# Performance work log

Measured on AMD Instinct MI355X. Metric: run time of the kernel, lower is better.

## Reference

```python
import jax, jax.numpy as jnp
import numpy as np

SH_DIM = 9                      # (sh_deg+1)^2, sh_deg=2
DATA_DIM = SH_DIM * 3 + 1       # 28
FINE = 8
COARSE = 32
RADIUS = 1.3
NUM_ATOMS = 16
BATCH = 128
STEP = (RADIUS * 2.0 / COARSE / FINE) / 2.0   # fine_voxel_len / 2
N_INTRS = COARSE * 3 * 2 * FINE               # 1536


def sh_encode(dirs):
    # degree-2 real spherical harmonics bases, [.., 9]
    x, y, z = dirs[..., 0], dirs[..., 1], dirs[..., 2]
    C0 = 0.28209479177387814
    C1 = 0.4886025119029199
    C2 = (1.0925484305920792, -1.0925484305920792, 0.31539156525252005,
          -1.0925484305920792, 0.5462742152960396)
    return jnp.stack([
        jnp.full_like(x, C0), -C1 * y, C1 * z, -C1 * x,
        C2[0] * x * y, C2[1] * y * z, C2[2] * (2.0 * z * z - x * x - y * y),
        C2[3] * x * z, C2[4] * (x * x - y * y)], axis=-1)


def dict_interp(grid, atoms, pts):
    # pts: [N,3] normalized to [0,1). grid: [COARSE^3, A]. atoms: [FINE^3, A, D].
    # coarse voxel -> dictionary coefficients; trilinear interp of atoms inside it.
    cpos = pts * COARSE
    cidx = jnp.clip(jnp.floor(cpos), 0, COARSE - 1)
    ci = cidx.astype(jnp.int32)
    coeff = grid[(ci[:, 0] * COARSE + ci[:, 1]) * COARSE + ci[:, 2]]  # [N, A]
    local = cpos - cidx                       # [0,1) within coarse voxel
    fpos = local * FINE - 0.5
    f0f = jnp.floor(fpos)
    w = fpos - f0f                            # trilinear weights
    f0 = f0f.astype(jnp.int32)
    out = jnp.zeros((pts.shape[0], DATA_DIM), dtype=pts.dtype)
    for dx in (0, 1):
        for dy in (0, 1):
            for dz in (0, 1):
                ix = jnp.clip(f0[:, 0] + dx, 0, FINE - 1)
                iy = jnp.clip(f0[:, 1] + dy, 0, FINE - 1)
                iz = jnp.clip(f0[:, 2] + dz, 0, FINE - 1)
                wt = ((w[:, 0] if dx else 1.0 - w[:, 0]) *
                      (w[:, 1] if dy else 1.0 - w[:, 1]) *
                      (w[:, 2] if dz else 1.0 - w[:, 2]))
                vals = jnp.einsum('na,nad->nd', coeff, atoms[(ix * FINE + iy) * FINE + iz])
                out = out + wt[:, None] * vals
    return out


def setup_inputs() -> dict:
    key = jax.random.key(0)
    k1, k2, k3, k4 = jax.random.split(key, 4)
    rays_o = jnp.array([0.0, 0.0, -2.0 * RADIUS]) + 0.05 * jax.random.normal(k1, (BATCH, 3), jnp.float32)
    d = 0.25 * jax.random.normal(k2, (BATCH, 3), jnp.float32) + jnp.array([0.0, 0.0, 1.0])
    rays_d = d / jnp.linalg.norm(d, axis=-1, keepdims=True)
    grid = 0.01 * jax.random.normal(k3, (COARSE ** 3, NUM_ATOMS), jnp.float32)
    atoms_sh = jax.random.uniform(k4, (FINE ** 3, NUM_ATOMS, DATA_DIM - 1), jnp.float32)
    atoms = jnp.concatenate([atoms_sh, jnp.full((FINE ** 3, NUM_ATOMS, 1), 0.01, jnp.float32)], -1)
    return {"rays_o": rays_o, "rays_d": rays_d, "grid": grid, "atoms": atoms, "grid_id": 0}


def reference(rays_o, rays_d, grid, atoms, grid_id):
    B = rays_o.shape[0]
    # ---- sample_proposal (no-grad in original) ----
    off_pos = (RADIUS - rays_o) / rays_d
    off_neg = (-RADIUS - rays_o) / rays_d
    start = jnp.max(jnp.minimum(off_pos, off_neg), axis=-1, keepdims=True)
    steps = jnp.arange(N_INTRS, dtype=rays_o.dtype)[None, :]
    intersections = jax.lax.stop_gradient(start + steps * STEP)        # [B, 1536]
    tsec = intersections[:, :-1]                                       # [B, M]
    M = N_INTRS - 1
    pts = rays_o[:, None, :] + tsec[:, :, None] * rays_d[:, None, :]   # [B, M, 3]
    mask = jnp.all((pts > -RADIUS) & (pts < RADIUS), axis=-1)          # [B, M]
    pts_n = jnp.clip((pts + RADIUS) / (2.0 * RADIUS), 0.0, 1.0 - 1e-6)
    pts_n = jax.lax.stop_gradient(pts_n).reshape(-1, 3)
    # ---- dictionary interpolation (computed densely, zeroed by mask) ----
    data = dict_interp(grid, atoms, pts_n).reshape(B, M, DATA_DIM)
    sigma = jax.nn.relu(jnp.where(mask, data[..., -1], 0.0))           # [B, M]
    # ---- sigma -> alpha / weights ----
    dists = (intersections[:, 1:] - intersections[:, :-1]) * jnp.linalg.norm(rays_d, axis=-1, keepdims=True)
    alpha = 1.0 - jnp.exp(-sigma * dists)
    trans = jnp.concatenate([jnp.ones((B, 1), alpha.dtype),
                             jnp.cumprod(1.0 - alpha + 1e-10, axis=-1)[:, :-1]], axis=-1)
    abs_light = alpha * trans                                          # [B, M]
    # ---- SH -> rgb, composite ----
    sh_mult = sh_encode(rays_d)[:, None, None, :]                      # [B,1,1,9]
    sh = data[..., :-1].reshape(B, M, 3, SH_DIM)
    rgb_raw = jnp.where(mask[..., None], jnp.sum(sh_mult * sh, axis=-1), 0.0)  # [B,M,3]
    rgb = jnp.sum(abs_light[..., None] * jax.nn.sigmoid(rgb_raw), axis=1)
    rgb = rgb + (1.0 - jnp.sum(abs_light, axis=-1))[:, None]           # white background
    depth = jnp.sum(abs_light * tsec, axis=-1)
    return rgb, alpha, depth
```

## Files before the change

### kernel.cpp

```cpp
#include <hip/hip_runtime.h>

typedef unsigned int u32;

#define MSAMP 1535
#define NS 1024
#define RADF 1.3f
#define STEPF ((float)(1.3 * 2.0 / 32.0 / 8.0 / 2.0))
#define NATOMS 229376
#define NCELLG 32768
#define CSCALE 0.06f

#if __has_builtin(__builtin_amdgcn_sdot4)
#define SDOT4(a, b, c) __builtin_amdgcn_sdot4((a), (b), (c), false)
#else
static __device__ __forceinline__ int SDOT4(int a, int b, int c) {
#pragma unroll
    for (int i = 0; i < 4; i++) {
        int ai = (a << (24 - 8 * i)) >> 24;
        int bi = (b << (24 - 8 * i)) >> 24;
        c += ai * bi;
    }
    return c;
}
#endif

__device__ __forceinline__ u32 q4(float a, float b, float c, float d, float S) {
    int i0 = (int)rintf(fminf(fmaxf(a * S, -127.0f), 127.0f));
    int i1 = (int)rintf(fminf(fmaxf(b * S, -127.0f), 127.0f));
    int i2 = (int)rintf(fminf(fmaxf(c * S, -127.0f), 127.0f));
    int i3 = (int)rintf(fminf(fmaxf(d * S, -127.0f), 127.0f));
    return (u32)(i0 & 255) | ((u32)(i1 & 255) << 8) | ((u32)(i2 & 255) << 16)
         | ((u32)(i3 & 255) << 24);
}

__global__ __launch_bounds__(256) void k_t(const float* __restrict__ atoms,
                                           const float* __restrict__ grid,
                                           signed char* __restrict__ wst2,
                                           uint4* __restrict__ gridq,
                                           float4* __restrict__ acc4) {
    int o = blockIdx.x * 256 + threadIdx.x;
    if (o < NATOMS) {
        float v = atoms[o];
        int cell = o / 448;
        int r = o - cell * 448;
        int a = r / 28;
        int d = r - a * 28;
        int s = d >> 2, j = d & 3;
        int qv = (int)rintf(v * 127.0f);
        wst2[s * 32768 + cell * 64 + j * 16 + a] = (signed char)qv;
    } else if (o < NATOMS + NCELLG) {
        int cell = o - NATOMS;
        const float4* gp = (const float4*)(grid + cell * 16);
        float4 c0 = gp[0], c1 = gp[1], c2 = gp[2], c3 = gp[3];
        const float S = 127.0f / CSCALE;
        uint4 outv;
        outv.x = q4(c0.x, c0.y, c0.z, c0.w, S);
        outv.y = q4(c1.x, c1.y, c1.z, c1.w, S);
        outv.z = q4(c2.x, c2.y, c2.z, c2.w, S);
        outv.w = q4(c3.x, c3.y, c3.z, c3.w, S);
        gridq[cell] = outv;
    } else {
        acc4[o - NATOMS - NCELLG] = make_float4(0.0f, 0.0f, 0.0f, 0.0f);
    }
}

__global__ __launch_bounds__(512) void k_p1(const float* __restrict__ ro,
                                            const float* __restrict__ rd,
                                            const uint4* __restrict__ gridq,
                                            const signed char* __restrict__ wst2,
                                            float* __restrict__ acc4) {
    __shared__ __align__(16) signed char hl[512 * 80];
    int bx = blockIdx.x;
    int s  = bx >> 6;
    int pr = bx & 63;
    int tid = threadIdx.x;
    int ray = pr * 2 + (tid >> 8);
    int q   = tid & 255;

    {
        const uint4* src = (const uint4*)(wst2 + s * 32768);
#pragma unroll
        for (int it = 0; it < 4; it++) {
            int idx = it * 512 + tid;
            uint4 v = src[idx];
            int cell = idx >> 2, part = idx & 3;
            *(uint4*)&hl[cell * 80 + part * 16] = v;
        }
    }
    __syncthreads();

    float ox = ro[ray * 3 + 0], oy = ro[ray * 3 + 1], oz = ro[ray * 3 + 2];
    float dx = rd[ray * 3 + 0], dy = rd[ray * 3 + 1], dz = rd[ray * 3 + 2];
    float a0 = ( RADF - ox) / dx, b0 = (-RADF - ox) / dx;
    float a1 = ( RADF - oy) / dy, b1 = (-RADF - oy) / dy;
    float a2 = ( RADF - oz) / dz, b2 = (-RADF - oz) / dz;
    float st = fmaxf(fmaxf(fminf(a0, b0), fminf(a1, b1)), fminf(a2, b2));

    float shm[9];
    shm[0] = 0.28209479177387814f;
    shm[1] = -0.4886025119029199f * dy;
    shm[2] =  0.4886025119029199f * dz;
    shm[3] = -0.4886025119029199f * dx;
    shm[4] =  1.0925484305920792f * dx * dy;
    shm[5] = -1.0925484305920792f * dy * dz;
    shm[6] =  0.31539156525252005f * (2.0f * dz * dz - dx * dx - dy * dy);
    shm[7] = -1.0925484305920792f * dx * dz;
    shm[8] =  0.5462742152960396f * (dx * dx - dy * dy);

    float wA[4] = {0,0,0,0}, wB[4] = {0,0,0,0};
    int chanA = 0, chanB = 0; bool hasB = false;
    switch (s) {
        case 0: chanA=0; wA[0]=shm[0]; wA[1]=shm[1]; wA[2]=shm[2]; wA[3]=shm[3]; break;
        case 1: chanA=0; wA[0]=shm[4]; wA[1]=shm[5]; wA[2]=shm[6]; wA[3]=shm[7]; break;
        case 2: chanA=0; wA[0]=shm[8];
                chanB=1; wB[1]=shm[0]; wB[2]=shm[1]; wB[3]=shm[2]; hasB=true; break;
        case 3: chanA=1; wA[0]=shm[3]; wA[1]=shm[4]; wA[2]=shm[5]; wA[3]=shm[6]; break;
        case 4: chanA=1; wA[0]=shm[7]; wA[1]=shm[8];
                chanB=2; wB[2]=shm[0]; wB[3]=shm[1]; hasB=true; break;
        case 5: chanA=2; wA[0]=shm[2]; wA[1]=shm[3]; wA[2]=shm[4]; wA[3]=shm[5]; break;
        default: chanA=2; wA[0]=shm[6]; wA[1]=shm[7]; wA[2]=shm[8];
                chanB=3; wB[3]=1.0f; hasB=true; break;
    }
    const float QS = CSCALE / (127.0f * 127.0f);
#pragma unroll
    for (int i = 0; i < 4; i++) { wA[i] *= QS; wB[i] *= QS; }

#pragma unroll
    for (int k = 0; k < 4; k++) {
        int m = q + k * 256;
        float t = st + (float)m * STEPF;
        float px = ox + t * dx, py = oy + t * dy, pz = oz + t * dz;
        bool inb = (px > -RADF) && (px < RADF) && (py > -RADF) && (py < RADF)
                && (pz > -RADF) && (pz < RADF);
        if (!inb) continue;

        const float inv2R = 1.0f / 2.6f;
        float pnx = fminf(fmaxf((px + RADF) * inv2R, 0.0f), 0.999999f);
        float pny = fminf(fmaxf((py + RADF) * inv2R, 0.0f), 0.999999f);
        float pnz = fminf(fmaxf((pz + RADF) * inv2R, 0.0f), 0.999999f);

        float cpx = pnx * 32.0f, cpy = pny * 32.0f, cpz = pnz * 32.0f;
        float cfx = floorf(cpx), cfy = floorf(cpy), cfz = floorf(cpz);
        int cix = (int)cfx, ciy = (int)cfy, ciz = (int)cfz;

        float fpx = (cpx - cfx) * 8.0f - 0.5f;
        float fpy = (cpy - cfy) * 8.0f - 0.5f;
        float fpz = (cpz - cfz) * 8.0f - 0.5f;
        float ffx = floorf(fpx), ffy = floorf(fpy), ffz = floorf(fpz);
        int f0x = (int)ffx, f0y = (int)ffy, f0z = (int)ffz;
        float wx = fpx - ffx, wy = fpy - ffy, wz = fpz - ffz;

        int ixa[2] = { max(f0x, 0), min(f0x + 1, 7) };
        int iya[2] = { max(f0y, 0), min(f0y + 1, 7) };
        int iza[2] = { max(f0z, 0), min(f0z + 1, 7) };
        float wxa[2] = { 1.0f - wx, wx };
        float wya[2] = { 1.0f - wy, wy };
        float wza[2] = { 1.0f - wz, wz };

        uint4 cq = gridq[(cix * 32 + ciy) * 32 + ciz];
        float acc[4] = {0.0f, 0.0f, 0.0f, 0.0f};

#pragma unroll
        for (int cx = 0; cx < 2; cx++)
#pragma unroll
        for (int cy = 0; cy < 2; cy++)
#pragma unroll
        for (int cz = 0; cz < 2; cz++) {
            float wt = wxa[cx] * wya[cy] * wza[cz];
            int cb = ((ixa[cx] * 8 + iya[cy]) * 8 + iza[cz]) * 80;
#pragma unroll
            for (int j = 0; j < 4; j++) {
                uint4 qa = *(const uint4*)&hl[cb + j * 16];
                int di = SDOT4((int)qa.x, (int)cq.x, 0);
                di = SDOT4((int)qa.y, (int)cq.y, di);
                di = SDOT4((int)qa.z, (int)cq.z, di);
                di = SDOT4((int)qa.w, (int)cq.w, di);
                acc[j] = fmaf(wt, (float)di, acc[j]);
            }
        }

        float vA = fmaf(wA[0], acc[0], fmaf(wA[1], acc[1],
                   fmaf(wA[2], acc[2], wA[3] * acc[3])));
        int base = (ray * NS + m) * 4;
        atomicAdd(&acc4[base + chanA], vA);
        if (hasB) {
            float vB = fmaf(wB[0], acc[0], fmaf(wB[1], acc[1],
                       fmaf(wB[2], acc[2], wB[3] * acc[3])));
            atomicAdd(&acc4[base + chanB], vB);
        }
    }
}

__global__ __launch_bounds__(1024) void k_p2(const float* __restrict__ ro,
                                             const float* __restrict__ rd,
                                             const float4* __restrict__ acc4,
                                             float* __restrict__ rgb_out,
                                             float* __restrict__ alpha_out,
                                             float* __restrict__ depth_out) {
    int ray = blockIdx.x;
    int t = threadIdx.x;
    int lane = t & 63, wave = t >> 6;

    int abase = ray * MSAMP;
    if (NS + t < MSAMP) alpha_out[abase + NS + t] = 0.0f;

    float dx = rd[ray * 3 + 0], dy = rd[ray * 3 + 1], dz = rd[ray * 3 + 2];
    float ox = ro[ray * 3 + 0], oy = ro[ray * 3 + 1], oz = ro[ray * 3 + 2];
    float a0 = ( RADF - ox) / dx, b0 = (-RADF - ox) / dx;
    float a1 = ( RADF - oy) / dy, b1 = (-RADF - oy) / dy;
    float a2 = ( RADF - oz) / dz, b2 = (-RADF - oz) / dz;
    float st = fmaxf(fmaxf(fminf(a0, b0), fminf(a1, b1)), fminf(a2, b2));
    float nrm = sqrtf(dx * dx + dy * dy + dz * dz);

    int m = t;
    float tm = st + (float)m * STEPF;
    float4 d4 = acc4[ray * NS + m];
    float sigma = fmaxf(d4.w, 0.0f);
    float alpha = 1.0f - __expf(-sigma * STEPF * nrm);
    float r0 = 1.0f / (1.0f + __expf(-d4.x));
    float r1 = 1.0f / (1.0f + __expf(-d4.y));
    float r2 = 1.0f / (1.0f + __expf(-d4.z));
    alpha_out[abase + m] = alpha;

    float p = 1.0f - alpha + 1e-10f;

    float incl = p;
#pragma unroll
    for (int off = 1; off < 64; off <<= 1) {
        float vv = __shfl_up(incl, off);
        if (lane >= off) incl *= vv;
    }
    __shared__ float wprod[16];
    if (lane == 63) wprod[wave] = incl;
    __syncthreads();
    float excl = __shfl_up(incl, 1);
    if (lane == 0) excl = 1.0f;
    for (int w = 0; w < 16; w++) if (w < wave) excl *= wprod[w];

    float w_ = alpha * excl;
    float vals[5] = { w_ * r0, w_ * r1, w_ * r2, w_ * tm, w_ };
    __shared__ float wred[16][5];
#pragma unroll
    for (int i = 0; i < 5; i++) {
        float v = vals[i];
        v += __shfl_xor(v, 1);  v += __shfl_xor(v, 2);  v += __shfl_xor(v, 4);
        v += __shfl_xor(v, 8);  v += __shfl_xor(v, 16); v += __shfl_xor(v, 32);
        if (lane == 0) wred[wave][i] = v;
    }
    __syncthreads();
    if (t == 0) {
        float res[5];
#pragma unroll
        for (int i = 0; i < 5; i++) {
            float r_ = 0.0f;
            for (int w = 0; w < 16; w++) r_ += wred[w][i];
            res[i] = r_;
        }
        float omw = 1.0f - res[4];
        rgb_out[ray * 3 + 0] = res[0] + omw;
        rgb_out[ray * 3 + 1] = res[1] + omw;
        rgb_out[ray * 3 + 2] = res[2] + omw;
        depth_out[ray] = res[3];
    }
}

extern "C" void kernel_launch(void* const* d_in, const int* in_sizes, int n_in,
                              void* d_out, int out_size, void* d_ws, size_t ws_size,
                              hipStream_t stream) {
    const float* ro    = (const float*)d_in[0];
    const float* rd    = (const float*)d_in[1];
    const float* grid  = (const float*)d_in[2];
    const float* atoms = (const float*)d_in[3];
    int B = in_sizes[0] / 3;

    signed char* wst2 = (signed char*)d_ws;
    uint4* gridq = (uint4*)((char*)d_ws + 229376);
    float* acc4  = (float*)((char*)d_ws + 229376 + 524288);

    float* out       = (float*)d_out;
    float* rgb_out   = out;
    float* alpha_out = out + B * 3;
    float* depth_out = out + B * 3 + B * MSAMP;

    hipLaunchKernelGGL(k_t,  dim3(393216 / 256), dim3(256), 0, stream,
                       atoms, grid, wst2, (uint4*)gridq, (float4*)acc4);
    hipLaunchKernelGGL(k_p1, dim3(448), dim3(512), 0, stream,
                       ro, rd, (const uint4*)gridq, wst2, acc4);
    hipLaunchKernelGGL(k_p2, dim3(B), dim3(1024), 0, stream,
                       ro, rd, (const float4*)acc4, rgb_out, alpha_out, depth_out);
}
```

Before: 83.17 us.

## Fold per-ray SH projection into atoms and fuse interpolation with compositing

New measurement: 74.84 us. 1.11x faster.

```diff
diff --git a/kernel.cpp b/kernel.cpp
--- a/kernel.cpp
+++ b/kernel.cpp
@@ -6,9 +6,9 @@
 #define NS 1024
 #define RADF 1.3f
 #define STEPF ((float)(1.3 * 2.0 / 32.0 / 8.0 / 2.0))
-#define NATOMS 229376
 #define NCELLG 32768
 #define CSCALE 0.06f
+#define PRANGE 4.0f
 
 #if __has_builtin(__builtin_amdgcn_sdot4)
 #define SDOT4(a, b, c) __builtin_amdgcn_sdot4((a), (b), (c), false)
@@ -33,23 +33,55 @@
          | ((u32)(i3 & 255) << 24);
 }
 
-__global__ __launch_bounds__(256) void k_t(const float* __restrict__ atoms,
-                                           const float* __restrict__ grid,
-                                           signed char* __restrict__ wst2,
-                                           uint4* __restrict__ gridq,
-                                           float4* __restrict__ acc4) {
-    int o = blockIdx.x * 256 + threadIdx.x;
-    if (o < NATOMS) {
-        float v = atoms[o];
-        int cell = o / 448;
-        int r = o - cell * 448;
-        int a = r / 28;
-        int d = r - a * 28;
-        int s = d >> 2, j = d & 3;
-        int qv = (int)rintf(v * 127.0f);
-        wst2[s * 32768 + cell * 64 + j * 16 + a] = (signed char)qv;
-    } else if (o < NATOMS + NCELLG) {
-        int cell = o - NATOMS;
+__global__ __launch_bounds__(256) void k_prep(const float* __restrict__ rd,
+                                              const float* __restrict__ atoms,
+                                              const float* __restrict__ grid,
+                                              uint4* __restrict__ Pq,
+                                              uint4* __restrict__ gridq) {
+    __shared__ __align__(16) float af[448];
+    int b = blockIdx.x, t = threadIdx.x;
+    if (b < 512) {
+        if (t < 112) ((float4*)af)[t] = ((const float4*)(atoms + b * 448))[t];
+        int r = t & 127;
+        float dx = rd[r * 3 + 0], dy = rd[r * 3 + 1], dz = rd[r * 3 + 2];
+        float shm[9];
+        shm[0] = 0.28209479177387814f;
+        shm[1] = -0.4886025119029199f * dy;
+        shm[2] =  0.4886025119029199f * dz;
+        shm[3] = -0.4886025119029199f * dx;
+        shm[4] =  1.0925484305920792f * dx * dy;
+        shm[5] = -1.0925484305920792f * dy * dz;
+        shm[6] =  0.31539156525252005f * (2.0f * dz * dz - dx * dx - dy * dy);
+        shm[7] = -1.0925484305920792f * dx * dz;
+        shm[8] =  0.5462742152960396f * (dx * dx - dy * dy);
+        __syncthreads();
+#pragma unroll
+        for (int iter = 0; iter < 2; iter++) {
+            int ch = (t >> 7) + 2 * iter;
+            u32 w[4] = {0u, 0u, 0u, 0u};
+            if (ch < 3) {
+                const float S = 127.0f / PRANGE;
+#pragma unroll
+                for (int a = 0; a < 16; a++) {
+                    const float* ap = af + a * 28 + ch * 9;
+                    float p = shm[0] * ap[0];
+#pragma unroll
+                    for (int k = 1; k < 9; k++) p = fmaf(shm[k], ap[k], p);
+                    int q = (int)rintf(fminf(fmaxf(p * S, -127.0f), 127.0f));
+                    w[a >> 2] |= ((u32)(q & 255)) << (8 * (a & 3));
+                }
+            } else {
+#pragma unroll
+                for (int a = 0; a < 16; a++) {
+                    float p = af[a * 28 + 27];
+                    int q = (int)rintf(fminf(fmaxf(p * 127.0f, -127.0f), 127.0f));
+                    w[a >> 2] |= ((u32)(q & 255)) << (8 * (a & 3));
+                }
+            }
+            Pq[b * 512 + r * 4 + ch] = make_uint4(w[0], w[1], w[2], w[3]);
+        }
+    } else {
+        int cell = (b - 512) * 256 + t;
         const float4* gp = (const float4*)(grid + cell * 16);
         float4 c0 = gp[0], c1 = gp[1], c2 = gp[2], c3 = gp[3];
         const float S = 127.0f / CSCALE;
@@ -59,35 +91,33 @@
         outv.z = q4(c2.x, c2.y, c2.z, c2.w, S);
         outv.w = q4(c3.x, c3.y, c3.z, c3.w, S);
         gridq[cell] = outv;
-    } else {
-        acc4[o - NATOMS - NCELLG] = make_float4(0.0f, 0.0f, 0.0f, 0.0f);
-    }
-}
-
-__global__ __launch_bounds__(512) void k_p1(const float* __restrict__ ro,
-                                            const float* __restrict__ rd,
-                                            const uint4* __restrict__ gridq,
-                                            const signed char* __restrict__ wst2,
-                                            float* __restrict__ acc4) {
+    }
+}
+
+__global__ __launch_bounds__(1024) void k_main(const float* __restrict__ ro,
+                                               const float* __restrict__ rd,
+                                               const uint4* __restrict__ gridq,
+                                               const uint4* __restrict__ Pq,
+                                               float* __restrict__ rgb_out,
+                                               float* __restrict__ alpha_out,
+                                               float* __restrict__ depth_out) {
     __shared__ __align__(16) signed char hl[512 * 80];
-    int bx = blockIdx.x;
-    int s  = bx >> 6;
-    int pr = bx & 63;
-    int tid = threadIdx.x;
-    int ray = pr * 2 + (tid >> 8);
-    int q   = tid & 255;
-
-    {
-        const uint4* src = (const uint4*)(wst2 + s * 32768);
-#pragma unroll
-        for (int it = 0; it < 4; it++) {
-            int idx = it * 512 + tid;
-            uint4 v = src[idx];
-            int cell = idx >> 2, part = idx & 3;
-            *(uint4*)&hl[cell * 80 + part * 16] = v;
-        }
-    }
-    __syncthreads();
+    __shared__ float wprod[16];
+    __shared__ float wred[16][5];
+    int ray = blockIdx.x;
+    int t = threadIdx.x;
+    int lane = t & 63, wave = t >> 6;
+
+#pragma unroll
+    for (int i = 0; i < 2; i++) {
+        int idx = i * 1024 + t;
+        int cell = idx >> 2, part = idx & 3;
+        uint4 v = Pq[cell * 512 + ray * 4 + part];
+        *(uint4*)&hl[cell * 80 + part * 16] = v;
+    }
+
+    int abase = ray * MSAMP;
+    if (NS + t < MSAMP) alpha_out[abase + NS + t] = 0.0f;
 
     float ox = ro[ray * 3 + 0], oy = ro[ray * 3 + 1], oz = ro[ray * 3 + 2];
     float dx = rd[ray * 3 + 0], dy = rd[ray * 3 + 1], dz = rd[ray * 3 + 2];
@@ -95,45 +125,17 @@
     float a1 = ( RADF - oy) / dy, b1 = (-RADF - oy) / dy;
     float a2 = ( RADF - oz) / dz, b2 = (-RADF - oz) / dz;
     float st = fmaxf(fmaxf(fminf(a0, b0), fminf(a1, b1)), fminf(a2, b2));
-
-    float shm[9];
-    shm[0] = 0.28209479177387814f;
-    shm[1] = -0.4886025119029199f * dy;
-    shm[2] =  0.4886025119029199f * dz;
-    shm[3] = -0.4886025119029199f * dx;
-    shm[4] =  1.0925484305920792f * dx * dy;
-    shm[5] = -1.0925484305920792f * dy * dz;
-    shm[6] =  0.31539156525252005f * (2.0f * dz * dz - dx * dx - dy * dy);
-    shm[7] = -1.0925484305920792f * dx * dz;
-    shm[8] =  0.5462742152960396f * (dx * dx - dy * dy);
-
-    float wA[4] = {0,0,0,0}, wB[4] = {0,0,0,0};
-    int chanA = 0, chanB = 0; bool hasB = false;
-    switch (s) {
-        case 0: chanA=0; wA[0]=shm[0]; wA[1]=shm[1]; wA[2]=shm[2]; wA[3]=shm[3]; break;
-        case 1: chanA=0; wA[0]=shm[4]; wA[1]=shm[5]; wA[2]=shm[6]; wA[3]=shm[7]; break;
-        case 2: chanA=0; wA[0]=shm[8];
-                chanB=1; wB[1]=shm[0]; wB[2]=shm[1]; wB[3]=shm[2]; hasB=true; break;
-        case 3: chanA=1; wA[0]=shm[3]; wA[1]=shm[4]; wA[2]=shm[5]; wA[3]=shm[6]; break;
-        case 4: chanA=1; wA[0]=shm[7]; wA[1]=shm[8];
-                chanB=2; wB[2]=shm[0]; wB[3]=shm[1]; hasB=true; break;
-        case 5: chanA=2; wA[0]=shm[2]; wA[1]=shm[3]; wA[2]=shm[4]; wA[3]=shm[5]; break;
-        default: chanA=2; wA[0]=shm[6]; wA[1]=shm[7]; wA[2]=shm[8];
-                chanB=3; wB[3]=1.0f; hasB=true; break;
-    }
-    const float QS = CSCALE / (127.0f * 127.0f);
-#pragma unroll
-    for (int i = 0; i < 4; i++) { wA[i] *= QS; wB[i] *= QS; }
-
-#pragma unroll
-    for (int k = 0; k < 4; k++) {
-        int m = q + k * 256;
-        float t = st + (float)m * STEPF;
-        float px = ox + t * dx, py = oy + t * dy, pz = oz + t * dz;
-        bool inb = (px > -RADF) && (px < RADF) && (py > -RADF) && (py < RADF)
-                && (pz > -RADF) && (pz < RADF);
-        if (!inb) continue;
-
+    float nrm = sqrtf(dx * dx + dy * dy + dz * dz);
+
+    __syncthreads();
+
+    float tm = st + (float)t * STEPF;
+    float px = ox + tm * dx, py = oy + tm * dy, pz = oz + tm * dz;
+    bool inb = (px > -RADF) && (px < RADF) && (py > -RADF) && (py < RADF)
+            && (pz > -RADF) && (pz < RADF);
+
+    float acc[4] = {0.0f, 0.0f, 0.0f, 0.0f};
+    if (inb) {
         const float inv2R = 1.0f / 2.6f;
         float pnx = fminf(fmaxf((px + RADF) * inv2R, 0.0f), 0.999999f);
         float pny = fminf(fmaxf((py + RADF) * inv2R, 0.0f), 0.999999f);
@@ -158,7 +160,6 @@
         float wza[2] = { 1.0f - wz, wz };
 
         uint4 cq = gridq[(cix * 32 + ciy) * 32 + ciz];
-        float acc[4] = {0.0f, 0.0f, 0.0f, 0.0f};
 
 #pragma unroll
         for (int cx = 0; cx < 2; cx++)
@@ -178,59 +179,24 @@
                 acc[j] = fmaf(wt, (float)di, acc[j]);
             }
         }
-
-        float vA = fmaf(wA[0], acc[0], fmaf(wA[1], acc[1],
-                   fmaf(wA[2], acc[2], wA[3] * acc[3])));
-        int base = (ray * NS + m) * 4;
-        atomicAdd(&acc4[base + chanA], vA);
-        if (hasB) {
-            float vB = fmaf(wB[0], acc[0], fmaf(wB[1], acc[1],
-                       fmaf(wB[2], acc[2], wB[3] * acc[3])));
-            atomicAdd(&acc4[base + chanB], vB);
-        }
-    }
-}
-
-__global__ __launch_bounds__(1024) void k_p2(const float* __restrict__ ro,
-                                             const float* __restrict__ rd,
-                                             const float4* __restrict__ acc4,
-                                             float* __restrict__ rgb_out,
-                                             float* __restrict__ alpha_out,
-                                             float* __restrict__ depth_out) {
-    int ray = blockIdx.x;
-    int t = threadIdx.x;
-    int lane = t & 63, wave = t >> 6;
-
-    int abase = ray * MSAMP;
-    if (NS + t < MSAMP) alpha_out[abase + NS + t] = 0.0f;
-
-    float dx = rd[ray * 3 + 0], dy = rd[ray * 3 + 1], dz = rd[ray * 3 + 2];
-    float ox = ro[ray * 3 + 0], oy = ro[ray * 3 + 1], oz = ro[ray * 3 + 2];
-    float a0 = ( RADF - ox) / dx, b0 = (-RADF - ox) / dx;
-    float a1 = ( RADF - oy) / dy, b1 = (-RADF - oy) / dy;
-    float a2 = ( RADF - oz) / dz, b2 = (-RADF - oz) / dz;
-    float st = fmaxf(fmaxf(fminf(a0, b0), fminf(a1, b1)), fminf(a2, b2));
-    float nrm = sqrtf(dx * dx + dy * dy + dz * dz);
-
-    int m = t;
-    float tm = st + (float)m * STEPF;
-    float4 d4 = acc4[ray * NS + m];
-    float sigma = fmaxf(d4.w, 0.0f);
+    }
+
+    const float QSC = CSCALE / (127.0f * 127.0f);
+    const float RSC = QSC * PRANGE;
+    float sigma = fmaxf(acc[3] * QSC, 0.0f);
     float alpha = 1.0f - __expf(-sigma * STEPF * nrm);
-    float r0 = 1.0f / (1.0f + __expf(-d4.x));
-    float r1 = 1.0f / (1.0f + __expf(-d4.y));
-    float r2 = 1.0f / (1.0f + __expf(-d4.z));
-    alpha_out[abase + m] = alpha;
+    float r0 = 1.0f / (1.0f + __expf(-acc[0] * RSC));
+    float r1 = 1.0f / (1.0f + __expf(-acc[1] * RSC));
+    float r2 = 1.0f / (1.0f + __expf(-acc[2] * RSC));
+    alpha_out[abase + t] = alpha;
 
     float p = 1.0f - alpha + 1e-10f;
-
     float incl = p;
 #pragma unroll
     for (int off = 1; off < 64; off <<= 1) {
         float vv = __shfl_up(incl, off);
         if (lane >= off) incl *= vv;
     }
-    __shared__ float wprod[16];
     if (lane == 63) wprod[wave] = incl;
     __syncthreads();
     float excl = __shfl_up(incl, 1);
@@ -239,7 +205,6 @@
 
     float w_ = alpha * excl;
     float vals[5] = { w_ * r0, w_ * r1, w_ * r2, w_ * tm, w_ };
-    __shared__ float wred[16][5];
 #pragma unroll
     for (int i = 0; i < 5; i++) {
         float v = vals[i];
@@ -273,19 +238,17 @@
     const float* atoms = (const float*)d_in[3];
     int B = in_sizes[0] / 3;
 
-    signed char* wst2 = (signed char*)d_ws;
-    uint4* gridq = (uint4*)((char*)d_ws + 229376);
-    float* acc4  = (float*)((char*)d_ws + 229376 + 524288);
+    uint4* gridq = (uint4*)d_ws;
+    uint4* Pq    = (uint4*)((char*)d_ws + 524288);
 
     float* out       = (float*)d_out;
     float* rgb_out   = out;
     float* alpha_out = out + B * 3;
     float* depth_out = out + B * 3 + B * MSAMP;
 
-    hipLaunchKernelGGL(k_t,  dim3(393216 / 256), dim3(256), 0, stream,
-                       atoms, grid, wst2, (uint4*)gridq, (float4*)acc4);
-    hipLaunchKernelGGL(k_p1, dim3(448), dim3(512), 0, stream,
-                       ro, rd, (const uint4*)gridq, wst2, acc4);
-    hipLaunchKernelGGL(k_p2, dim3(B), dim3(1024), 0, stream,
-                       ro, rd, (const float4*)acc4, rgb_out, alpha_out, depth_out);
-}
+    hipLaunchKernelGGL(k_prep, dim3(640), dim3(256), 0, stream,
+                       rd, atoms, grid, Pq, gridq);
+    hipLaunchKernelGGL(k_main, dim3(B), dim3(1024), 0, stream,
+                       ro, rd, (const uint4*)gridq, (const uint4*)Pq,
+                       rgb_out, alpha_out, depth_out);
+}
```
